# Performance work log

Hardware: AMD Instinct MI355X
Metric: run time of the kernel (lower is better)

## Reference

```python
import jax, jax.numpy as jnp
import numpy as np

DIM = 1024
DIM_HEAD = 64
HEADS = 16
INNER = DIM_HEAD * HEADS
SCALE = 8.0
EPS_LN = 1e-5
EPS_L2 = 1e-12


def _layernorm(x, gamma):
    mu = jnp.mean(x, axis=-1, keepdims=True)
    var = jnp.var(x, axis=-1, keepdims=True)
    return (x - mu) / jnp.sqrt(var + EPS_LN) * gamma  # beta is a zero buffer


def _l2norm(t):
    n = jnp.linalg.norm(t, axis=-1, keepdims=True)
    return t / jnp.maximum(n, EPS_L2)


def setup_inputs() -> dict:
    key = jax.random.key(0)
    ks = jax.random.split(key, 8)
    b, n = 4, 2048
    x = jax.random.normal(ks[0], (b, n, DIM), dtype=jnp.float32)
    context_mask = jax.random.randint(ks[1], (b, n), 0, 2) > 0
    gamma = jnp.ones((DIM,), dtype=jnp.float32)
    wq = jax.random.normal(ks[2], (DIM, INNER), dtype=jnp.float32) * 0.02
    wkv = jax.random.normal(ks[3], (DIM, 2 * INNER), dtype=jnp.float32) * 0.02
    null_kv = jax.random.normal(ks[4], (2, HEADS, 1, DIM_HEAD), dtype=jnp.float32)
    q_scale = jnp.ones((DIM_HEAD,), dtype=jnp.float32)
    k_scale = jnp.ones((DIM_HEAD,), dtype=jnp.float32)
    wo = jax.random.normal(ks[5], (INNER, DIM), dtype=jnp.float32) * 0.02
    return {"x": x, "context_mask": context_mask, "gamma": gamma, "wq": wq,
            "wkv": wkv, "null_kv": null_kv, "q_scale": q_scale,
            "k_scale": k_scale, "wo": wo}


def reference(x, context_mask, gamma, wq, wkv, null_kv, q_scale, k_scale, wo):
    b, n, _ = x.shape
    xn = _layernorm(x, gamma)
    q = xn @ wq                     # [b, n, inner]
    kv = xn @ wkv                   # self-attention: kv_input = x
    k, v = jnp.split(kv, 2, axis=-1)

    def split_heads(t):
        return t.reshape(b, n, HEADS, DIM_HEAD).transpose(0, 2, 1, 3)  # b h n d

    q, k, v = map(split_heads, (q, k, v))
    nk = jnp.broadcast_to(null_kv[0][None], (b, HEADS, 1, DIM_HEAD))
    nv = jnp.broadcast_to(null_kv[1][None], (b, HEADS, 1, DIM_HEAD))
    k = jnp.concatenate([nk, k], axis=2)  # b h (n+1) d
    v = jnp.concatenate([nv, v], axis=2)

    q = _l2norm(q) * q_scale
    k = _l2norm(k) * k_scale

    sim = jnp.einsum('bhid,bhjd->bhij', q, k) * SCALE  # b h n (n+1)
    mask = jnp.pad(context_mask, ((0, 0), (1, 0)), constant_values=True)  # null kv always visible
    mask_value = -jnp.finfo(sim.dtype).max
    sim = jnp.where(mask[:, None, None, :], sim, mask_value)

    attn = jax.nn.softmax(sim, axis=-1)
    out = jnp.einsum('bhij,bhjd->bhid', attn, v)
    out = out.transpose(0, 2, 1, 3).reshape(b, n, INNER)
    return out @ wo
```

## Files before the change

### kernel.cpp

```cpp
#include <hip/hip_runtime.h>

typedef unsigned short u16;
typedef unsigned int u32;
typedef unsigned long long u64;
typedef __bf16 bf16x8 __attribute__((ext_vector_type(8)));
typedef float f32x4 __attribute__((ext_vector_type(4)));

#define B_ 4
#define N_ 2048
#define D_ 1024
#define H_ 16
#define DH_ 64
#define NKP_ 2112
#define NKT_ 33

__device__ __forceinline__ float bf2f(u16 u) {
  union { u32 i; float f; } v; v.i = ((u32)u) << 16; return v.f;
}
__device__ __forceinline__ u16 f2bf(float f) {
  union { float f; u32 i; } v; v.f = f;
  u32 r = v.i + 0x7fffu + ((v.i >> 16) & 1u);
  return (u16)(r >> 16);
}
__device__ __forceinline__ u32 cvtpk(float a, float b) {
  u32 r;
  asm("v_cvt_pk_bf16_f32 %0, %1, %2" : "=v"(r) : "v"(a), "v"(b));
  return r;
}
__device__ __forceinline__ void load_lds16(const void* g, void* l) {
  __builtin_amdgcn_global_load_lds((const __attribute__((address_space(1))) void*)g,
                                   (__attribute__((address_space(3))) void*)l, 16, 0, 0);
}

__global__ __launch_bounds__(256) void ln_kernel(const float* __restrict__ x,
                                                 const float* __restrict__ gamma,
                                                 u16* __restrict__ xn) {
  int row = blockIdx.x;
  int tid = threadIdx.x, lane = tid & 63, wid = tid >> 6;
  const float4 v = ((const float4*)(x + (size_t)row * D_))[tid];
  float s  = v.x + v.y + v.z + v.w;
  float ss = v.x * v.x + v.y * v.y + v.z * v.z + v.w * v.w;
#pragma unroll
  for (int off = 1; off < 64; off <<= 1) {
    s  += __shfl_xor(s,  off, 64);
    ss += __shfl_xor(ss, off, 64);
  }
  __shared__ float rs[4], rss[4];
  if (lane == 0) { rs[wid] = s; rss[wid] = ss; }
  __syncthreads();
  float S  = rs[0] + rs[1] + rs[2] + rs[3];
  float SS = rss[0] + rss[1] + rss[2] + rss[3];
  float mean = S * (1.0f / D_);
  float var  = SS * (1.0f / D_) - mean * mean;
  float inv  = rsqrtf(var + 1e-5f);
  const float4 g = ((const float4*)gamma)[tid];
  ushort4 o;
  o.x = f2bf((v.x - mean) * inv * g.x);
  o.y = f2bf((v.y - mean) * inv * g.y);
  o.z = f2bf((v.z - mean) * inv * g.z);
  o.w = f2bf((v.w - mean) * inv * g.w);
  *(ushort4*)(xn + (size_t)row * D_ + tid * 4) = o;
}

__global__ __launch_bounds__(256) void wt_kernel(const float* __restrict__ W,
                                                 u16* __restrict__ WT,
                                                 int K, int N) {
  __shared__ float t[32][33];
  int tiles_n = N >> 5;
  int tk = blockIdx.x / tiles_n, tn = blockIdx.x % tiles_n;
  int tx = threadIdx.x & 31, ty = threadIdx.x >> 5;
  int k0 = tk << 5, n0 = tn << 5;
#pragma unroll
  for (int i = 0; i < 4; ++i)
    t[ty + i * 8][tx] = W[(size_t)(k0 + ty + i * 8) * N + n0 + tx];
  __syncthreads();
#pragma unroll
  for (int i = 0; i < 4; ++i)
    WT[(size_t)(n0 + ty + i * 8) * K + k0 + tx] = f2bf(t[tx][ty + i * 8]);
}

__global__ __launch_bounds__(256) void prep_kernel(const int* __restrict__ mask,
                                                   const float* __restrict__ qs,
                                                   const float* __restrict__ ksc,
                                                   const float* __restrict__ null_kv,
                                                   u16* __restrict__ Kb,
                                                   u16* __restrict__ Vt,
                                                   float* __restrict__ cb) {
  __shared__ int cnts[4];
  int bh = blockIdx.x, h = bh & 15;
  int tid = threadIdx.x, lane = tid & 63, wid = tid >> 6;
  if (wid == 0) {
    float kv = null_kv[h * 64 + lane];
    float ss = kv * kv;
#pragma unroll
    for (int off = 1; off < 64; off <<= 1) ss += __shfl_xor(ss, off, 64);
    float inv = 1.0f / fmaxf(sqrtf(ss), 1e-12f);
    Kb[((size_t)bh * NKP_ + 2048) * 64 + lane] = f2bf(kv * inv * ksc[lane]);
    Vt[((size_t)bh * 64 + lane) * NKP_ + 2048] = f2bf(null_kv[1024 + h * 64 + lane]);
  }
  for (int i = tid; i < 63 * 64; i += 256) {
    int r = i >> 6, c = i & 63;
    Kb[((size_t)bh * NKP_ + 2049 + r) * 64 + c] = 0;
  }
  for (int i = tid; i < 64 * 63; i += 256) {
    int d = i / 63, c = i % 63;
    Vt[((size_t)bh * 64 + d) * NKP_ + 2049 + c] = 0;
  }
  if (bh == 0) {
    if (tid < 4) cnts[tid] = 0;
    __syncthreads();
    int c0 = 0, c1 = 0, c2 = 0, c3 = 0;
    for (int i = tid; i < B_ * N_; i += 256) {
      int z = (mask[i] == 0);
      int b = i >> 11;
      if (b == 0) c0 += z; else if (b == 1) c1 += z; else if (b == 2) c2 += z; else c3 += z;
    }
    atomicAdd(&cnts[0], c0); atomicAdd(&cnts[1], c1);
    atomicAdd(&cnts[2], c2); atomicAdd(&cnts[3], c3);
    __syncthreads();
    if (tid == 0) {
      float mw = 0.f;
      for (int i = 0; i < DH_; ++i) mw = fmaxf(mw, fabsf(qs[i] * ksc[i]));
      float cbias = -8.0f * mw * 1.4426950408889634f;
      cb[0] = cbias;
      float e = __builtin_amdgcn_exp2f(cbias);
#pragma unroll
      for (int b = 0; b < 4; ++b) cb[1 + b] = (float)(cnts[b] + 63) * e;
    }
  }
}

__global__ __launch_bounds__(512, 1) void gemm_qkv(const u16* __restrict__ A,
                                                   const u16* __restrict__ Bt,
                                                   u16* __restrict__ Qo,
                                                   u16* __restrict__ Kb,
                                                   u16* __restrict__ Vt,
                                                   const float* __restrict__ qs,
                                                   const float* __restrict__ ksc,
                                                   const int* __restrict__ Mask) {
  __shared__ __attribute__((aligned(16))) u16 dsm[65536];
  int bx = blockIdx.x, by = blockIdx.y;
  int tid = threadIdx.x, lane = tid & 63, wid = tid >> 6;
  int wr = wid >> 2, wc = wid & 3;
  int m0 = bx * 256, n0 = by * 256;
  int wm = wr * 128, wn = wc * 64;
  int la = lane & 15, crow = (lane >> 4) * 4;
  int rq = lane >> 2;
  int scz32 = (((lane & 3) ^ ((lane >> 3) & 3))) * 8;
  int swzoff = (((lane >> 4) ^ ((la >> 1) & 3))) * 8;
  f32x4 acc[8][4] = {};

#define STAGE32(buf, kt)                                                       \
  do {                                                                         \
    int k0_ = (kt) * 32;                                                       \
    u16* ab_ = dsm + (buf) * 16384;                                            \
    _Pragma("unroll")                                                          \
    for (int i_ = 0; i_ < 2; ++i_) {                                           \
      int rb_ = i_ * 128 + wid * 16;                \
      load_lds16(A  + (size_t)(m0 + rb_ + rq) * 1024 + k0_ + scz32, ab_ + rb_ * 32); \
      load_lds16(Bt + (size_t)(n0 + rb_ + rq) * 1024 + k0_ + scz32, ab_ + 8192 + rb_ * 32); \
    }                                                                          \
  } while (0)

  STAGE32(0, 0);
  STAGE32(1, 1);
  STAGE32(2, 2);

  for (int t = 0; t < 32; ++t) {
    int buf = t & 3;
    __builtin_amdgcn_s_barrier();
    if (t + 3 < 32) {
      STAGE32((t + 3) & 3, t + 3);
      asm volatile("s_waitcnt vmcnt(12)" ::: "memory");
    } else if (t == 29) {
      asm volatile("s_waitcnt vmcnt(8)" ::: "memory");
    } else if (t == 30) {
      asm volatile("s_waitcnt vmcnt(4)" ::: "memory");
    } else {
      asm volatile("s_waitcnt vmcnt(0)" ::: "memory");
    }
    __builtin_amdgcn_s_barrier();
    __builtin_amdgcn_sched_barrier(0);

    const u16* a_l = dsm + buf * 16384;
    const u16* b_l = a_l + 8192;
    __builtin_amdgcn_s_setprio(1);
    bf16x8 bfr[4];
#pragma unroll
    for (int nf = 0; nf < 4; ++nf)
      bfr[nf] = *(const bf16x8*)&b_l[(wn + nf * 16 + la) * 32 + swzoff];
#pragma unroll
    for (int mf = 0; mf < 8; ++mf) {
      bf16x8 af = *(const bf16x8*)&a_l[(wm + mf * 16 + la) * 32 + swzoff];
#pragma unroll
      for (int nf = 0; nf < 4; ++nf)
        acc[mf][nf] = __builtin_amdgcn_mfma_f32_16x16x32_bf16(af, bfr[nf], acc[mf][nf], 0, 0, 0);
    }
    __builtin_amdgcn_s_setprio(0);
  }
#undef STAGE32

  int ccol = la;
  if (by < 4) {
    float qsv[4];
#pragma unroll
    for (int nf = 0; nf < 4; ++nf) qsv[nf] = qs[nf * 16 + ccol];
#pragma unroll
    for (int mf = 0; mf < 8; ++mf) {
      float invr[4];
#pragma unroll
      for (int r = 0; r < 4; ++r) {
        float ss = 0.f;
#pragma unroll
        for (int nf = 0; nf < 4; ++nf) ss += acc[mf][nf][r] * acc[mf][nf][r];
#pragma unroll
        for (int off = 1; off < 16; off <<= 1) ss += __shfl_xor(ss, off, 64);
        invr[r] = 1.0f / fmaxf(sqrtf(ss), 1e-12f);
      }
#pragma unroll
      for (int nf = 0; nf < 4; ++nf) {
        int rr = m0 + wm + mf * 16 + crow;
        int cc = by * 256 + wn + nf * 16 + ccol;
#pragma unroll
        for (int r = 0; r < 4; ++r)
          Qo[(size_t)(rr + r) * 1024 + cc] = f2bf(acc[mf][nf][r] * invr[r] * qsv[nf]);
      }
    }
    return;
  }

  int rr0 = m0 + wm;
  int b = rr0 >> 11;
  int seq0 = rr0 & 2047;
  const int* mrow = Mask + b * N_ + seq0;
  if (by < 8) {
    int h = (by - 4) * 4 + wc;
    float kscv[4];
#pragma unroll
    for (int nf = 0; nf < 4; ++nf) kscv[nf] = ksc[nf * 16 + ccol];
    u16* kb = Kb + ((size_t)(b * 16 + h) * NKP_) * 64;
#pragma unroll
    for (int mf = 0; mf < 8; ++mf) {
      float invr[4]; int mvv[4];
#pragma unroll
      for (int r = 0; r < 4; ++r) {
        float ss = 0.f;
#pragma unroll
        for (int nf = 0; nf < 4; ++nf) ss += acc[mf][nf][r] * acc[mf][nf][r];
#pragma unroll
        for (int off = 1; off < 16; off <<= 1) ss += __shfl_xor(ss, off, 64);
        invr[r] = 1.0f / fmaxf(sqrtf(ss), 1e-12f);
        mvv[r] = mrow[mf * 16 + crow + r];
      }
#pragma unroll
      for (int nf = 0; nf < 4; ++nf)
#pragma unroll
        for (int r = 0; r < 4; ++r)
          kb[(size_t)(seq0 + mf * 16 + crow + r) * 64 + nf * 16 + ccol] =
              f2bf(mvv[r] ? acc[mf][nf][r] * invr[r] * kscv[nf] : 0.f);
    }
  } else {
    int h = (by - 8) * 4 + wc;
    __syncthreads();
    u16* tw = dsm + wid * 8192;
#pragma unroll
    for (int mf = 0; mf < 8; ++mf) {
      int mvv[4];
#pragma unroll
      for (int r = 0; r < 4; ++r) mvv[r] = mrow[mf * 16 + crow + r];
#pragma unroll
      for (int nf = 0; nf < 4; ++nf) {
        int d = nf * 16 + ccol;
#pragma unroll
        for (int r = 0; r < 4; ++r) {
          int key = mf * 16 + crow + r;
          tw[d * 128 + ((((key >> 3) ^ (d & 7)) << 3) | (key & 7))] =
              f2bf(mvv[r] ? acc[mf][nf][r] : 0.f);
        }
      }
    }
    u16* vb = Vt + ((size_t)(b * 16 + h) * 64) * NKP_;
    int key0 = seq0;
    int dr = lane >> 3, kc8 = (lane & 7);
#pragma unroll
    for (int j = 0; j < 8; ++j) {
      int d = j * 8 + dr;
#pragma unroll
      for (int half = 0; half < 2; ++half) {
        int kslot = kc8 + half * 8;
        bf16x8 vv = *(const bf16x8*)&tw[d * 128 + (((kslot ^ (d & 7)) & 15) * 8)];
        *(bf16x8*)(vb + (size_t)d * NKP_ + key0 + kslot * 8) = vv;
      }
    }
  }
}

#define GEMM_BODY(A, Bt)                                                       \
  int tid = threadIdx.x, lane = tid & 63, wid = tid >> 6;                      \
  int m0 = blockIdx.x * 128, n0 = blockIdx.y * 128;                            \
  int wm = (wid >> 1) * 64, wn = (wid & 1) * 64;                               \
  int sr = lane >> 3;                                                          \
  int scz = ((lane & 7) ^ (lane >> 3)) * 8;                                    \
  int la = lane & 15, lk = (lane >> 4) * 8;                                    \
  int swz = (la & 7) * 8;                                                      \
  f32x4 acc[4][4] = {};                                                        \
  for (int kt = 0; kt < 16; ++kt) {                                            \
    int k0_ = kt * 64;                                                         \
    __syncthreads();                                                           \
    _Pragma("unroll")                                                          \
    for (int i_ = 0; i_ < 4; ++i_) {                                           \
      int r_ = i_ * 32 + wid * 8;                                              \
      load_lds16(A + (size_t)(m0 + r_ + sr) * 1024 + k0_ + scz, &a_sm[r_ * 64]); \
      load_lds16(Bt + (size_t)(n0 + r_ + sr) * 1024 + k0_ + scz, &b_sm[r_ * 64]); \
    }                                                                          \
    __syncthreads();                                                           \
    _Pragma("unroll")                                                          \
    for (int s = 0; s < 2; ++s) {                                              \
      bf16x8 af[4], bfr[4];                                                    \
      _Pragma("unroll")                                                        \
      for (int mf = 0; mf < 4; ++mf)                                           \
        af[mf] = *(const bf16x8*)&a_sm[(wm + mf * 16 + la) * 64 + ((s * 32 + lk) ^ swz)]; \
      _Pragma("unroll")                                                        \
      for (int nf = 0; nf < 4; ++nf)                                           \
        bfr[nf] = *(const bf16x8*)&b_sm[(wn + nf * 16 + la) * 64 + ((s * 32 + lk) ^ swz)]; \
      _Pragma("unroll")                                                        \
      for (int mf = 0; mf < 4; ++mf)                                           \
        _Pragma("unroll")                                                      \
        for (int nf = 0; nf < 4; ++nf)                                         \
          acc[mf][nf] = __builtin_amdgcn_mfma_f32_16x16x32_bf16(af[mf], bfr[nf], acc[mf][nf], 0, 0, 0); \
    }                                                                          \
  }                                                                            \
  int crow = (lane >> 4) * 4, ccol = lane & 15;

__global__ __launch_bounds__(256) void gemm_out(const u16* __restrict__ A,
                                                const u16* __restrict__ Bt,
                                                float* __restrict__ C) {
  __shared__ __attribute__((aligned(16))) u16 sm[2 * 128 * 64];
  u16* a_sm = sm;
  u16* b_sm = sm + 128 * 64;
  GEMM_BODY(A, Bt)
#pragma unroll
  for (int mf = 0; mf < 4; ++mf)
#pragma unroll
    for (int nf = 0; nf < 4; ++nf) {
      int rr = m0 + wm + mf * 16 + crow;
      int cc = n0 + wn + nf * 16 + ccol;
#pragma unroll
      for (int r = 0; r < 4; ++r) C[(size_t)(rr + r) * 1024 + cc] = acc[mf][nf][r];
    }
}

__global__ __launch_bounds__(512) void attn_kernel(const u16* __restrict__ Q,
                                                   const u16* __restrict__ Kb,
                                                   const u16* __restrict__ Vt,
                                                   const float* __restrict__ cb,
                                                   u16* __restrict__ O) {
  __shared__ __attribute__((aligned(16))) u16 k_sm[2][64 * 64];
  __shared__ __attribute__((aligned(16))) u16 v_sm[2][64 * 64];
  __shared__ __attribute__((aligned(16))) u16 p_sm[8][32 * 64];
  int tid = threadIdx.x, lane = tid & 63, wid = tid >> 6;
  int bh = blockIdx.x, b = bh >> 4, h = bh & 15;
  int q0 = blockIdx.y * 256 + wid * 32;
  int la = lane & 15, lk = (lane >> 4) * 8, crow = (lane >> 4) * 4;
  int swz = (la & 7) * 8;
  int sr = lane >> 3;
  int scz = ((lane & 7) ^ (lane >> 3)) * 8;

  bf16x8 aq[2][2];
#pragma unroll
  for (int qb = 0; qb < 2; ++qb) {
    const u16* qrow = Q + ((size_t)(b * N_) + q0 + qb * 16 + la) * D_ + h * DH_;
#pragma unroll
    for (int s = 0; s < 2; ++s) aq[qb][s] = *(const bf16x8*)(qrow + s * 32 + lk);
  }
  float l[2] = {0.f, 0.f};
  f32x4 o[2][4] = {};
  const u16* Kbh = Kb + (size_t)bh * NKP_ * 64;
  const u16* Vbh = Vt + (size_t)bh * 64 * NKP_;
  const float C1 = 11.541560327111707f;
  const float cbias = cb[0];
  const float lsub = cb[1 + b];

#define STAGE(bb, kt)                                                          \
  do {                                                                         \
    int key0_ = (kt) * 64;                                                     \
    int r_ = wid * 8;                                                          \
    load_lds16(Kbh + (size_t)(key0_ + r_ + sr) * 64 + scz, &k_sm[bb][r_ * 64]); \
    load_lds16(Vbh + (size_t)(r_ + sr) * NKP_ + key0_ + scz, &v_sm[bb][r_ * 64]); \
  } while (0)

  STAGE(0, 0);

#pragma unroll 2
  for (int kt = 0; kt < NKT_; ++kt) {
    int bb = kt & 1;
    __syncthreads();
    if (kt + 1 < NKT_) STAGE(bb ^ 1, kt + 1);

    f32x4 sacc[2][4] = {};
    __builtin_amdgcn_s_setprio(1);
#pragma unroll
    for (int nf = 0; nf < 4; ++nf) {
      bf16x8 bk0 = *(const bf16x8*)&k_sm[bb][(nf * 16 + la) * 64 + (lk ^ swz)];
      bf16x8 bk1 = *(const bf16x8*)&k_sm[bb][(nf * 16 + la) * 64 + ((32 + lk) ^ swz)];
#pragma unroll
      for (int qb = 0; qb < 2; ++qb) {
        sacc[qb][nf] = __builtin_amdgcn_mfma_f32_16x16x32_bf16(bk0, aq[qb][0], sacc[qb][nf], 0, 0, 0);
        sacc[qb][nf] = __builtin_amdgcn_mfma_f32_16x16x32_bf16(bk1, aq[qb][1], sacc[qb][nf], 0, 0, 0);
      }
    }
    __builtin_amdgcn_s_setprio(0);

#pragma unroll
    for (int nf = 0; nf < 4; ++nf) {
      int key = nf * 16 + crow;
#pragma unroll
      for (int qb = 0; qb < 2; ++qb) {
        float p0 = __builtin_amdgcn_exp2f(fmaf(sacc[qb][nf][0], C1, cbias));
        float p1 = __builtin_amdgcn_exp2f(fmaf(sacc[qb][nf][1], C1, cbias));
        float p2 = __builtin_amdgcn_exp2f(fmaf(sacc[qb][nf][2], C1, cbias));
        float p3 = __builtin_amdgcn_exp2f(fmaf(sacc[qb][nf][3], C1, cbias));
        l[qb] += (p0 + p1) + (p2 + p3);
        uint2 pw;
        pw.x = cvtpk(p0, p1);
        pw.y = cvtpk(p2, p3);
        *(uint2*)&p_sm[wid][(qb * 16 + la) * 64 + (key ^ swz)] = pw;
      }
    }

    __builtin_amdgcn_s_setprio(1);
#pragma unroll
    for (int s = 0; s < 2; ++s) {
      bf16x8 bv[4];
#pragma unroll
      for (int dt = 0; dt < 4; ++dt)
        bv[dt] = *(const bf16x8*)&v_sm[bb][(dt * 16 + la) * 64 + ((s * 32 + lk) ^ swz)];
#pragma unroll
      for (int qb = 0; qb < 2; ++qb) {
        bf16x8 ap = *(const bf16x8*)&p_sm[wid][(qb * 16 + la) * 64 + ((s * 32 + lk) ^ swz)];
#pragma unroll
        for (int dt = 0; dt < 4; ++dt)
          o[qb][dt] = __builtin_amdgcn_mfma_f32_16x16x32_bf16(ap, bv[dt], o[qb][dt], 0, 0, 0);
      }
    }
    __builtin_amdgcn_s_setprio(0);
  }
#undef STAGE

#pragma unroll
  for (int qb = 0; qb < 2; ++qb) {
    l[qb] += __shfl_xor(l[qb], 16, 64);
    l[qb] += __shfl_xor(l[qb], 32, 64);
#pragma unroll
    for (int r = 0; r < 4; ++r) {
      float lq = __shfl(l[qb], crow + r, 64) - lsub;
      float inv = 1.0f / lq;
      int n = q0 + qb * 16 + crow + r;
      u16* ob = O + ((size_t)(b * N_) + n) * D_ + h * DH_;
#pragma unroll
      for (int dt = 0; dt < 4; ++dt) ob[dt * 16 + la] = f2bf(o[qb][dt][r] * inv);
    }
  }
}

extern "C" void kernel_launch(void* const* d_in, const int* in_sizes, int n_in,
                              void* d_out, int out_size, void* d_ws, size_t ws_size,
                              hipStream_t stream) {
  (void)in_sizes; (void)n_in; (void)out_size; (void)ws_size;
  const float* x     = (const float*)d_in[0];
  const int*   mask  = (const int*)d_in[1];
  const float* gamma = (const float*)d_in[2];
  const float* wq    = (const float*)d_in[3];
  const float* wkv   = (const float*)d_in[4];
  const float* nkv   = (const float*)d_in[5];
  const float* qs    = (const float*)d_in[6];
  const float* ksc   = (const float*)d_in[7];
  const float* wo    = (const float*)d_in[8];

  char* ws   = (char*)d_ws;
  u16* xn    = (u16*)(ws);
  u16* wqkvT = (u16*)(ws + (16ull << 20));
  u16* wkvT  = wqkvT + 1024 * 1024;
  u16* woT   = (u16*)(ws + (22ull << 20));
  u16* Kb    = (u16*)(ws + (24ull << 20));
  u16* Vt    = (u16*)(ws + (41ull << 20));
  float* cb  = (float*)(ws + (58ull << 20));
  u16* q_tmp = (u16*)d_out;
  u16* attn_out = xn;

  ln_kernel<<<B_ * N_, 256, 0, stream>>>(x, gamma, xn);
  wt_kernel<<<(1024 / 32) * (1024 / 32), 256, 0, stream>>>(wq, wqkvT, 1024, 1024);
  wt_kernel<<<(1024 / 32) * (2048 / 32), 256, 0, stream>>>(wkv, wkvT, 1024, 2048);
  wt_kernel<<<(1024 / 32) * (1024 / 32), 256, 0, stream>>>(wo, woT, 1024, 1024);
  prep_kernel<<<64, 256, 0, stream>>>(mask, qs, ksc, nkv, Kb, Vt, cb);
  gemm_qkv<<<dim3(32, 12), 512, 0, stream>>>(xn, wqkvT, q_tmp, Kb, Vt, qs, ksc, mask);
  attn_kernel<<<dim3(64, 8), 512, 0, stream>>>(q_tmp, Kb, Vt, cb, attn_out);
  gemm_out<<<dim3(64, 8), 256, 0, stream>>>(attn_out, woT, (float*)d_out);
}
```

Before: 212.1 us.

## Halve QKV GEMM shared memory with double buffering to raise occupancy

Cuts the QKV projection kernel's LDS from 128KB to 64KB by moving from a 4-stage prefetch ring to a 2-stage double buffer. It raises the launch-bounds minimum blocks per CU to 4, so more blocks can be resident at once. The V-transpose epilogue now stages the 128-key tile in two 64-key halves so it fits the smaller buffer. In exchange, memory latency is hidden less deeply within each block. The 256x256 tile's large accumulator set may also spill under the tighter register budget that the new launch bounds imply.

```diff
diff --git a/kernel.cpp b/kernel.cpp
--- a/kernel.cpp
+++ b/kernel.cpp
@@ -130,7 +130,7 @@
   }
 }
 
-__global__ __launch_bounds__(512, 1) void gemm_qkv(const u16* __restrict__ A,
+__global__ __launch_bounds__(512, 4) void gemm_qkv(const u16* __restrict__ A,
                                                    const u16* __restrict__ Bt,
                                                    u16* __restrict__ Qo,
                                                    u16* __restrict__ Kb,
@@ -138,7 +138,7 @@
                                                    const float* __restrict__ qs,
                                                    const float* __restrict__ ksc,
                                                    const int* __restrict__ Mask) {
-  __shared__ __attribute__((aligned(16))) u16 dsm[65536];
+  __shared__ __attribute__((aligned(16))) u16 dsm[32768];
   int bx = blockIdx.x, by = blockIdx.y;
   int tid = threadIdx.x, lane = tid & 63, wid = tid >> 6;
   int wr = wid >> 2, wc = wid & 3;
@@ -163,18 +163,12 @@
   } while (0)
 
   STAGE32(0, 0);
-  STAGE32(1, 1);
-  STAGE32(2, 2);
 
   for (int t = 0; t < 32; ++t) {
-    int buf = t & 3;
+    int buf = t & 1;
     __builtin_amdgcn_s_barrier();
-    if (t + 3 < 32) {
-      STAGE32((t + 3) & 3, t + 3);
-      asm volatile("s_waitcnt vmcnt(12)" ::: "memory");
-    } else if (t == 29) {
-      asm volatile("s_waitcnt vmcnt(8)" ::: "memory");
-    } else if (t == 30) {
+    if (t + 1 < 32) {
+      STAGE32(buf ^ 1, t + 1);
       asm volatile("s_waitcnt vmcnt(4)" ::: "memory");
     } else {
       asm volatile("s_waitcnt vmcnt(0)" ::: "memory");
@@ -262,34 +256,32 @@
   } else {
     int h = (by - 8) * 4 + wc;
     __syncthreads();
-    u16* tw = dsm + wid * 8192;
-#pragma unroll
-    for (int mf = 0; mf < 8; ++mf) {
-      int mvv[4];
-#pragma unroll
-      for (int r = 0; r < 4; ++r) mvv[r] = mrow[mf * 16 + crow + r];
-#pragma unroll
-      for (int nf = 0; nf < 4; ++nf) {
-        int d = nf * 16 + ccol;
-#pragma unroll
-        for (int r = 0; r < 4; ++r) {
-          int key = mf * 16 + crow + r;
-          tw[d * 128 + ((((key >> 3) ^ (d & 7)) << 3) | (key & 7))] =
-              f2bf(mvv[r] ? acc[mf][nf][r] : 0.f);
+    u16* tw = dsm + wid * 4096;
+    u16* vb = Vt + ((size_t)(b * 16 + h) * 64) * NKP_;
+    int dr = lane >> 3, kc = (lane & 7) * 8;
+#pragma unroll
+    for (int h2 = 0; h2 < 2; ++h2) {
+#pragma unroll
+      for (int mf2 = 0; mf2 < 4; ++mf2) {
+        int mf = h2 * 4 + mf2;
+        int mvv[4];
+#pragma unroll
+        for (int r = 0; r < 4; ++r) mvv[r] = mrow[mf * 16 + crow + r];
+#pragma unroll
+        for (int nf = 0; nf < 4; ++nf) {
+          int d = nf * 16 + ccol;
+#pragma unroll
+          for (int r = 0; r < 4; ++r) {
+            int key = mf2 * 16 + crow + r;
+            tw[d * 64 + (key ^ ((d & 7) * 8))] = f2bf(mvv[r] ? acc[mf][nf][r] : 0.f);
+          }
         }
       }
-    }
-    u16* vb = Vt + ((size_t)(b * 16 + h) * 64) * NKP_;
-    int key0 = seq0;
-    int dr = lane >> 3, kc8 = (lane & 7);
-#pragma unroll
-    for (int j = 0; j < 8; ++j) {
-      int d = j * 8 + dr;
-#pragma unroll
-      for (int half = 0; half < 2; ++half) {
-        int kslot = kc8 + half * 8;
-        bf16x8 vv = *(const bf16x8*)&tw[d * 128 + (((kslot ^ (d & 7)) & 15) * 8)];
-        *(bf16x8*)(vb + (size_t)d * NKP_ + key0 + kslot * 8) = vv;
+#pragma unroll
+      for (int i = 0; i < 8; ++i) {
+        int d = i * 8 + dr;
+        bf16x8 vv = *(const bf16x8*)&tw[d * 64 + (kc ^ ((d & 7) * 8))];
+        *(bf16x8*)(vb + (size_t)d * NKP_ + seq0 + h2 * 64 + kc) = vv;
       }
     }
   }
```

Result: slower. 431.6 us (+103.5%).
